# Kernel optimization log

Measured on AMD Instinct MI355X. Metric: run time of the kernel, lower is better.

## Reference

```python
import jax, jax.numpy as jnp
import numpy as np

H, KVH, D = 32, 8, 128
HID = H * D
OP = H * D + 2 * KVH * D
T = 2048
LAYER_IDX = 8
LAMBDA_INIT = float(0.8 - 0.6 * np.exp(-0.3 * LAYER_IDX))
EPS = 1e-5


def setup_inputs() -> dict:
    key = jax.random.key(0)
    ks = jax.random.split(key, 10)
    s = 0.02
    return {
        "hidden_states": jax.random.normal(ks[0], (T, HID), jnp.float32),
        "wqkv_w": jax.random.normal(ks[1], (OP, HID), jnp.float32) * s,
        "wqkv_b": jax.random.normal(ks[2], (OP,), jnp.float32) * s,
        "lambda_q1": jax.random.normal(ks[3], (D,), jnp.float32) * 0.1,
        "lambda_k1": jax.random.normal(ks[4], (D,), jnp.float32) * 0.1,
        "lambda_q2": jax.random.normal(ks[5], (D,), jnp.float32) * 0.1,
        "lambda_k2": jax.random.normal(ks[6], (D,), jnp.float32) * 0.1,
        "subln_w": jnp.ones((2 * D,), jnp.float32),
        "out_w": jax.random.normal(ks[7], (HID, HID), jnp.float32) * s,
        "out_b": jax.random.normal(ks[8], (HID,), jnp.float32) * s,
    }


def reference(hidden_states, wqkv_w, wqkv_b, lambda_q1, lambda_k1,
              lambda_q2, lambda_k2, subln_w, out_w, out_b):
    t = hidden_states.shape[0]
    scale = D ** -0.5

    qkv = hidden_states @ wqkv_w.T + wqkv_b                     # [T, OP]
    q, k, v = jnp.split(qkv, [H * D, H * D + KVH * D], axis=-1)

    # pair-wise head split: consecutive heads form (pair, component) groups
    q = q.reshape(t, H // 2, 2, D)                              # [T, Hp, 2, D]
    k = k.reshape(t, KVH // 2, 2, D)                            # [T, KVHp, 2, D]
    v = v.reshape(t, KVH // 2, 2 * D)                           # [T, KVHp, 2D]

    rep = H // KVH  # GQA: query pair p -> kv pair p // rep
    k = jnp.repeat(k, rep, axis=1)                              # [T, Hp, 2, D]
    v = jnp.repeat(v, rep, axis=1)                              # [T, Hp, 2D]

    lam = (jnp.exp(jnp.dot(lambda_q1, lambda_k1))
           - jnp.exp(jnp.dot(lambda_q2, lambda_k2)) + LAMBDA_INIT)

    causal = jnp.tril(jnp.ones((t, t), bool))
    scores = jnp.einsum('qhcd,khcd->hcqk', q, k) * scale        # [Hp, 2, T, T]
    scores = jnp.where(causal, scores, -jnp.inf)
    probs = jax.nn.softmax(scores, axis=-1)
    attn = probs[:, 0] - lam * probs[:, 1]                      # [Hp, T, T]

    out = jnp.einsum('hqk,khd->qhd', attn, v)                   # [T, Hp, 2D]

    # per-head RMSNorm over 2D, scaled by (1 - lambda_init)
    rms = jax.lax.rsqrt(jnp.mean(out * out, axis=-1, keepdims=True) + EPS)
    out = out * rms * subln_w * (1.0 - LAMBDA_INIT)

    out = out.reshape(t, H * D)
    return out @ out_w.T + out_b
```

## Files before the change

kernel.cpp:

```cpp
#include <hip/hip_runtime.h>

#define TTOK 2048
#define HIDN 4096
#define OPD  6144
#define DH   128
#define VD   256
#define KOFF 4096
#define VOFF 5120

typedef short  s16x8 __attribute__((ext_vector_type(8)));
typedef unsigned short u16x8 __attribute__((ext_vector_type(8)));
typedef float  fx4   __attribute__((ext_vector_type(4)));

constexpr float LAM_INIT = 0.7455692280263534f;
constexpr float OML      = 1.0f - LAM_INIT;
constexpr float QKSCALE  = 0.08838834764831845f;
constexpr float RESCALE_THR = 8.0f;

__device__ __forceinline__ unsigned short f2bf(float f) {
  unsigned int u = __builtin_bit_cast(unsigned int, f);
  u += 0x7fffu + ((u >> 16) & 1u);
  return (unsigned short)(u >> 16);
}

__device__ __forceinline__ unsigned int cvtpk(float lo, float hi) {
  unsigned int r;
  asm("v_cvt_pk_bf16_f32 %0, %1, %2" : "=v"(r) : "v"(lo), "v"(hi));
  return r;
}

__device__ __forceinline__ void g2l16(const void* gsrc, void* ldst) {
  __builtin_amdgcn_global_load_lds(
      (const __attribute__((address_space(1))) unsigned int*)gsrc,
      (__attribute__((address_space(3))) unsigned int*)ldst, 16, 0, 0);
}

__global__ __launch_bounds__(256)
void cvt3(const float* __restrict__ s0, unsigned short* __restrict__ d0, int nb0,
          const float* __restrict__ s1, unsigned short* __restrict__ d1, int nb1,
          const float* __restrict__ s2, unsigned short* __restrict__ d2)
{
  const int b = blockIdx.x;
  const float* s; unsigned short* d; int base;
  if (b < nb0)            { s = s0; d = d0; base = b << 11; }
  else if (b < nb0 + nb1) { s = s1; d = d1; base = (b - nb0) << 11; }
  else                    { s = s2; d = d2; base = (b - nb0 - nb1) << 11; }
  const int i = base + (int)threadIdx.x * 8;
  const float4 a0 = *(const float4*)(s + i);
  const float4 a1 = *(const float4*)(s + i + 4);
  u16x8 v;
  v[0]=f2bf(a0.x); v[1]=f2bf(a0.y); v[2]=f2bf(a0.z); v[3]=f2bf(a0.w);
  v[4]=f2bf(a1.x); v[5]=f2bf(a1.y); v[6]=f2bf(a1.z); v[7]=f2bf(a1.w);
  *(u16x8*)(d + i) = v;
}

__global__ __launch_bounds__(256)
void reduce2(const float* __restrict__ p, const float* __restrict__ bias,
             float* __restrict__ out)
{
  const size_t i = ((size_t)blockIdx.x * 256 + threadIdx.x) * 4;
  const int col = (int)(i & (HIDN - 1));
  const float4 a = *(const float4*)(p + i);
  const float4 b = *(const float4*)(p + (size_t)TTOK * HIDN + i);
  const float4 c = *(const float4*)(bias + col);
  float4 r;
  r.x = a.x + b.x + c.x; r.y = a.y + b.y + c.y;
  r.z = a.z + b.z + c.z; r.w = a.w + b.w + c.w;
  *(float4*)(out + i) = r;
}

__global__ __launch_bounds__(512, 2)
void gemm1_qkv(const unsigned short* __restrict__ A, const unsigned short* __restrict__ B,
               const float* __restrict__ bias, unsigned short* __restrict__ qq,
               unsigned short* __restrict__ ctt)
{
  __shared__ __align__(16) unsigned short As[2][2][128 * 64];
  __shared__ __align__(16) unsigned short Bs[2][192 * 64];

  const int tid  = threadIdx.x;
  const int lane = tid & 63, wid = tid >> 6;
  const int wm = wid >> 1, wn = wid & 1;
  const int m0 = blockIdx.y * 256, n0 = blockIdx.x * 192;
  const int l15 = lane & 15, lg = lane >> 4;

  const int scol = ((tid & 7) ^ ((tid >> 3) & 7)) << 3;
  const int rsw = (l15 & 7) << 3;
  const int ck0 = (lg * 8) ^ rsw;
  const int ck1 = (32 + lg * 8) ^ rsw;
  const int arh = wm * 16 + l15;
  const int brh = wn * 96 + l15;

  auto stageAh = [&](int kt, int buf, int h) {
    #pragma unroll
    for (int i = 0; i < 2; ++i) {
      const int li = i * 512 + tid;
      g2l16(A + (size_t)(m0 + h * 128 + (li >> 3)) * HIDN + kt + scol,
            &As[buf][h][li * 8]);
    }
  };
  auto stageB = [&](int kt, int buf) {
    #pragma unroll
    for (int i = 0; i < 3; ++i) {
      const int li = i * 512 + tid;
      g2l16(B + (size_t)(n0 + (li >> 3)) * HIDN + kt + scol,
            &Bs[buf][li * 8]);
    }
  };

  fx4 acc[4][6] = {};

  const int nk = HIDN >> 6;
  stageAh(0, 0, 0); stageB(0, 0); stageAh(0, 0, 1);
  asm volatile("s_waitcnt vmcnt(0)" ::: "memory");
  __builtin_amdgcn_s_barrier();

  for (int t = 0; t < nk; ++t) {
    const int buf = t & 1, nb = buf ^ 1;
    const int kt1 = (t + 1) << 6;
    const bool pre = (t + 1) < nk;
    const unsigned short* A0 = &As[buf][0][0];
    const unsigned short* A1 = &As[buf][1][0];
    const unsigned short* Bp = &Bs[buf][0];
    s16x8 af[2], bk0[6], bk1[6];

    af[0] = *(const s16x8*)&A0[(arh)      * 64 + ck0];
    af[1] = *(const s16x8*)&A0[(arh + 64) * 64 + ck0];
    #pragma unroll
    for (int n = 0; n < 6; ++n)
      bk0[n] = *(const s16x8*)&Bp[(brh + n * 16) * 64 + ck0];
    if (pre) {
      stageAh(kt1, nb, 0);
      asm volatile("s_waitcnt vmcnt(2)" ::: "memory");
    } else {
      asm volatile("s_waitcnt vmcnt(0)" ::: "memory");
    }
    __builtin_amdgcn_s_barrier();
    __builtin_amdgcn_s_setprio(1);
    #pragma unroll
    for (int m = 0; m < 2; ++m)
      #pragma unroll
      for (int n = 0; n < 6; ++n)
        acc[m][n] = __builtin_amdgcn_mfma_f32_16x16x32_bf16(af[m], bk0[n], acc[m][n], 0, 0, 0);
    __builtin_amdgcn_s_setprio(0);

    af[0] = *(const s16x8*)&A0[(arh)      * 64 + ck1];
    af[1] = *(const s16x8*)&A0[(arh + 64) * 64 + ck1];
    #pragma unroll
    for (int n = 0; n < 6; ++n)
      bk1[n] = *(const s16x8*)&Bp[(brh + n * 16) * 64 + ck1];
    if (pre) stageB(kt1, nb);
    __builtin_amdgcn_s_barrier();
    __builtin_amdgcn_s_setprio(1);
    #pragma unroll
    for (int m = 0; m < 2; ++m)
      #pragma unroll
      for (int n = 0; n < 6; ++n)
        acc[m][n] = __builtin_amdgcn_mfma_f32_16x16x32_bf16(af[m], bk1[n], acc[m][n], 0, 0, 0);
    __builtin_amdgcn_s_setprio(0);

    af[0] = *(const s16x8*)&A1[(arh)      * 64 + ck0];
    af[1] = *(const s16x8*)&A1[(arh + 64) * 64 + ck0];
    if (pre) stageAh(kt1, nb, 1);
    __builtin_amdgcn_s_setprio(1);
    #pragma unroll
    for (int m = 0; m < 2; ++m)
      #pragma unroll
      for (int n = 0; n < 6; ++n)
        acc[2 + m][n] = __builtin_amdgcn_mfma_f32_16x16x32_bf16(af[m], bk0[n], acc[2 + m][n], 0, 0, 0);
    __builtin_amdgcn_s_setprio(0);

    af[0] = *(const s16x8*)&A1[(arh)      * 64 + ck1];
    af[1] = *(const s16x8*)&A1[(arh + 64) * 64 + ck1];
    __builtin_amdgcn_s_setprio(1);
    #pragma unroll
    for (int m = 0; m < 2; ++m)
      #pragma unroll
      for (int n = 0; n < 6; ++n)
        acc[2 + m][n] = __builtin_amdgcn_mfma_f32_16x16x32_bf16(af[m], bk1[n], acc[2 + m][n], 0, 0, 0);
    __builtin_amdgcn_s_setprio(0);
  }

  #pragma unroll
  for (int mi = 0; mi < 4; ++mi)
    #pragma unroll
    for (int ni = 0; ni < 6; ++ni) {
      const int colg = n0 + wn * 96 + ni * 16;
      const int col  = colg + l15;
      const float bv = bias[col];
      const fx4 a = acc[mi][ni];
      const int row0 = m0 + mi * 64 + wm * 16 + lg * 4;
      if (colg >= VOFF) {
        ushort4 pk;
        pk.x = f2bf(a[0] + bv); pk.y = f2bf(a[1] + bv);
        pk.z = f2bf(a[2] + bv); pk.w = f2bf(a[3] + bv);
        const int d = col - VOFF;
        const int kvp = d >> 8, dw = d & 255;
        const int kt2 = row0 >> 5, kk = row0 & 31;
        const int kc = kk >> 3, k8 = kk & 7;
        *(ushort4*)&ctt[(size_t)kvp * 1048576 + (size_t)kt2 * 16384 + 8192
                        + kc * 2048 + dw * 8 + k8] = pk;
      } else if (colg >= KOFF) {
        const int ccol = col - KOFF;
        const int kvp = ccol >> 8, cw = ccol & 255;
        const int cc = cw >> 3, cbt = cw & 7;
        #pragma unroll
        for (int jj = 0; jj < 4; ++jj) {
          const int row2 = row0 + jj;
          const int kt2 = row2 >> 5, kk = row2 & 31;
          ctt[(size_t)kvp * 1048576 + (size_t)kt2 * 16384 + cc * 256 + kk * 8 + cbt]
              = f2bf(a[jj] + bv);
        }
      } else {
        #pragma unroll
        for (int jj = 0; jj < 4; ++jj)
          qq[(size_t)(row0 + jj) * HIDN + col] = f2bf((a[jj] + bv) * QKSCALE);
      }
    }
}

__global__ __launch_bounds__(512, 2)
void gemm2_sk(const unsigned short* __restrict__ A, const unsigned short* __restrict__ B,
              float* __restrict__ P, int K, int lda, int ldb, int ldc)
{
  __shared__ __align__(16) unsigned short As[2][2][128 * 64];
  __shared__ __align__(16) unsigned short Bs[2][2][128 * 64];

  const int tid  = threadIdx.x;
  const int lane = tid & 63, wid = tid >> 6;
  const int wm = wid >> 2, wn = wid & 3;
  const int m0 = blockIdx.y * 256, n0 = blockIdx.x * 256;
  const int l15 = lane & 15, lg = lane >> 4;
  const int kOff = blockIdx.z * K;

  const int scol = ((tid & 7) ^ ((tid >> 3) & 7)) << 3;
  const int rsw = (l15 & 7) << 3;
  const int ck0 = (lg * 8) ^ rsw;
  const int ck1 = (32 + lg * 8) ^ rsw;
  const int arh = wm * 16 + l15;
  const int brh = wn * 16 + l15;

  auto stageAh = [&](int kt, int buf, int h) {
    #pragma unroll
    for (int i = 0; i < 2; ++i) {
      const int li = i * 512 + tid;
      g2l16(A + (size_t)(m0 + h * 128 + (li >> 3)) * lda + kOff + kt + scol,
            &As[buf][h][li * 8]);
    }
  };
  auto stageBh = [&](int kt, int buf, int h) {
    #pragma unroll
    for (int i = 0; i < 2; ++i) {
      const int li = i * 512 + tid;
      g2l16(B + (size_t)(n0 + h * 128 + (li >> 3)) * ldb + kOff + kt + scol,
            &Bs[buf][h][li * 8]);
    }
  };

  fx4 acc[8][4] = {};

  const int nk = K >> 6;
  stageAh(0, 0, 0); stageBh(0, 0, 0); stageBh(0, 0, 1); stageAh(0, 0, 1);
  asm volatile("s_waitcnt vmcnt(0)" ::: "memory");
  __builtin_amdgcn_s_barrier();

  for (int t = 0; t < nk; ++t) {
    const int buf = t & 1, nb = buf ^ 1;
    const int kt1 = (t + 1) << 6;
    const bool pre = (t + 1) < nk;
    const unsigned short* A0 = &As[buf][0][0];
    const unsigned short* A1 = &As[buf][1][0];
    const unsigned short* B0 = &Bs[buf][0][0];
    const unsigned short* B1 = &Bs[buf][1][0];
    s16x8 af[4][2], bf0[2][2], bf1[2][2];

    #pragma unroll
    for (int m = 0; m < 4; ++m) {
      af[m][0] = *(const s16x8*)&A0[(arh + m * 32) * 64 + ck0];
      af[m][1] = *(const s16x8*)&A0[(arh + m * 32) * 64 + ck1];
    }
    #pragma unroll
    for (int n = 0; n < 2; ++n) {
      bf0[n][0] = *(const s16x8*)&B0[(brh + n * 64) * 64 + ck0];
      bf0[n][1] = *(const s16x8*)&B0[(brh + n * 64) * 64 + ck1];
    }
    if (pre) {
      stageAh(kt1, nb, 0);
      asm volatile("s_waitcnt vmcnt(4)" ::: "memory");
    } else {
      asm volatile("s_waitcnt vmcnt(0)" ::: "memory");
    }
    __builtin_amdgcn_s_barrier();
    __builtin_amdgcn_s_setprio(1);
    #pragma unroll
    for (int m = 0; m < 4; ++m)
      #pragma unroll
      for (int n = 0; n < 2; ++n) {
        acc[m][n] = __builtin_amdgcn_mfma_f32_16x16x32_bf16(af[m][0], bf0[n][0], acc[m][n], 0, 0, 0);
        acc[m][n] = __builtin_amdgcn_mfma_f32_16x16x32_bf16(af[m][1], bf0[n][1], acc[m][n], 0, 0, 0);
      }
    __builtin_amdgcn_s_setprio(0);

    #pragma unroll
    for (int n = 0; n < 2; ++n) {
      bf1[n][0] = *(const s16x8*)&B1[(brh + n * 64) * 64 + ck0];
      bf1[n][1] = *(const s16x8*)&B1[(brh + n * 64) * 64 + ck1];
    }
    if (pre) {
      stageBh(kt1, nb, 0);
      asm volatile("s_waitcnt vmcnt(4)" ::: "memory");
    }
    __builtin_amdgcn_s_barrier();
    __builtin_amdgcn_s_setprio(1);
    #pragma unroll
    for (int m = 0; m < 4; ++m)
      #pragma unroll
      for (int n = 0; n < 2; ++n) {
        acc[m][2 + n] = __builtin_amdgcn_mfma_f32_16x16x32_bf16(af[m][0], bf1[n][0], acc[m][2 + n], 0, 0, 0);
        acc[m][2 + n] = __builtin_amdgcn_mfma_f32_16x16x32_bf16(af[m][1], bf1[n][1], acc[m][2 + n], 0, 0, 0);
      }
    __builtin_amdgcn_s_setprio(0);

    #pragma unroll
    for (int m = 0; m < 4; ++m) {
      af[m][0] = *(const s16x8*)&A1[(arh + m * 32) * 64 + ck0];
      af[m][1] = *(const s16x8*)&A1[(arh + m * 32) * 64 + ck1];
    }
    if (pre) stageBh(kt1, nb, 1);
    __builtin_amdgcn_s_setprio(1);
    #pragma unroll
    for (int m = 0; m < 4; ++m)
      #pragma unroll
      for (int n = 0; n < 2; ++n) {
        acc[4 + m][2 + n] = __builtin_amdgcn_mfma_f32_16x16x32_bf16(af[m][0], bf1[n][0], acc[4 + m][2 + n], 0, 0, 0);
        acc[4 + m][2 + n] = __builtin_amdgcn_mfma_f32_16x16x32_bf16(af[m][1], bf1[n][1], acc[4 + m][2 + n], 0, 0, 0);
      }
    __builtin_amdgcn_s_setprio(0);

    if (pre) stageAh(kt1, nb, 1);
    __builtin_amdgcn_s_setprio(1);
    #pragma unroll
    for (int m = 0; m < 4; ++m)
      #pragma unroll
      for (int n = 0; n < 2; ++n) {
        acc[4 + m][n] = __builtin_amdgcn_mfma_f32_16x16x32_bf16(af[m][0], bf0[n][0], acc[4 + m][n], 0, 0, 0);
        acc[4 + m][n] = __builtin_amdgcn_mfma_f32_16x16x32_bf16(af[m][1], bf0[n][1], acc[4 + m][n], 0, 0, 0);
      }
    __builtin_amdgcn_s_setprio(0);
    if (pre) asm volatile("s_waitcnt vmcnt(4)" ::: "memory");
    __builtin_amdgcn_s_barrier();
  }

  float* Pz = P + (size_t)blockIdx.z * TTOK * ldc;
  const int rb = m0 + wm * 16;
  const int cb = n0 + wn * 16;
  #pragma unroll
  for (int mi = 0; mi < 8; ++mi)
    #pragma unroll
    for (int ni = 0; ni < 4; ++ni) {
      const int col = cb + ni * 64 + l15;
      const fx4 a = acc[mi][ni];
      #pragma unroll
      for (int jj = 0; jj < 4; ++jj)
        Pz[(size_t)(rb + mi * 32 + lg * 4 + jj) * ldc + col] = a[jj];
    }
}

__global__ __launch_bounds__(256, 2)
void attn_kernel(const unsigned short* __restrict__ qq,
                 const unsigned short* __restrict__ ctt,
                 const float* __restrict__ lq1, const float* __restrict__ lk1,
                 const float* __restrict__ lq2, const float* __restrict__ lk2,
                 const float* __restrict__ subln,
                 unsigned short* __restrict__ attn_out)
{
  __shared__ __align__(16) unsigned short Sb[2][16384];
  __shared__ __align__(16) unsigned short Pl[4][2][640];
  const int tid = threadIdx.x;
  const int lane = tid & 63, w = tid >> 6;
  const int l15 = lane & 15, lg = lane >> 4;

  const int bid  = blockIdx.x;
  const int r    = bid & 255;
  const int pair = r & 15;
  const int x    = r >> 4;
  const int qb   = (bid >> 8) ? x : 31 - x;
  const int kvp  = pair >> 2;
  const int q0b  = qb * 64;
  const int q0w  = q0b + w * 16;
  const int nt   = 2 * qb + 2;

  const unsigned short* cbase = ctt + (size_t)kvp * 1048576;

  auto stage = [&](int kt, int buf) {
    const unsigned short* src = cbase + (size_t)kt * 16384;
    const int off = w * 512 + lane * 8;
    #pragma unroll
    for (int i = 0; i < 8; ++i) {
      const int o = i * 2048 + off;
      g2l16(src + o, &Sb[buf][o]);
    }
  };

  stage(0, 0);

  float a1 = lq1[lane] * lk1[lane] + lq1[lane + 64] * lk1[lane + 64];
  float a2 = lq2[lane] * lk2[lane] + lq2[lane + 64] * lk2[lane + 64];
  #pragma unroll
  for (int sft = 1; sft < 64; sft <<= 1) { a1 += __shfl_xor(a1, sft); a2 += __shfl_xor(a2, sft); }
  const float lam = __expf(a1) - __expf(a2) + LAM_INIT;

  s16x8 qf0[4], qf1[4];
  {
    const unsigned short* qbp = qq + (size_t)(q0w + l15) * HIDN + pair * VD + lg * 8;
    #pragma unroll
    for (int kf = 0; kf < 4; ++kf) {
      qf0[kf] = *(const s16x8*)(qbp + kf * 32);
      qf1[kf] = *(const s16x8*)(qbp + DH + kf * 32);
    }
  }

  float mrun0 = -1e30f, mrun1 = -1e30f;
  float lrun0 = 0.f, lrun1 = 0.f;
  fx4 oacc0[16] = {}, oacc1[16] = {};
  unsigned short* pl0 = &Pl[w][0][0];
  unsigned short* pl1 = &Pl[w][1][0];
  const int q = q0w + l15;
  const int qmax = q0w + 15;

  for (int t = 0; t < nt; ++t) {
    __syncthreads();
    if (t + 1 < nt) stage(t + 1, (t + 1) & 1);
    const int kb = t * 32;
    if (kb > qmax) continue;
    const unsigned short* Kl = Sb[t & 1];
    const unsigned short* Vl = Sb[t & 1] + 8192;

    fx4 s00 = {0,0,0,0}, s01 = {0,0,0,0}, s10 = {0,0,0,0}, s11 = {0,0,0,0};
    #pragma unroll
    for (int kf = 0; kf < 4; ++kf) {
      const int cc0 = kf * 4 + lg;
      const int cc1 = 16 + kf * 4 + lg;
      const s16x8 k00 = *(const s16x8*)&Kl[cc0 * 256 + l15 * 8];
      const s16x8 k01 = *(const s16x8*)&Kl[cc0 * 256 + (16 + l15) * 8];
      const s16x8 k10 = *(const s16x8*)&Kl[cc1 * 256 + l15 * 8];
      const s16x8 k11 = *(const s16x8*)&Kl[cc1 * 256 + (16 + l15) * 8];
      s00 = __builtin_amdgcn_mfma_f32_16x16x32_bf16(k00, qf0[kf], s00, 0, 0, 0);
      s01 = __builtin_amdgcn_mfma_f32_16x16x32_bf16(k01, qf0[kf], s01, 0, 0, 0);
      s10 = __builtin_amdgcn_mfma_f32_16x16x32_bf16(k10, qf1[kf], s10, 0, 0, 0);
      s11 = __builtin_amdgcn_mfma_f32_16x16x32_bf16(k11, qf1[kf], s11, 0, 0, 0);
    }

    float v0[8], v1[8];
    if (kb + 32 <= q0w) {
      #pragma unroll
      for (int j = 0; j < 4; ++j) {
        v0[j] = s00[j]; v0[4 + j] = s01[j];
        v1[j] = s10[j]; v1[4 + j] = s11[j];
      }
    } else {
      #pragma unroll
      for (int j = 0; j < 4; ++j) {
        const int klo = kb + lg * 4 + j, khi = klo + 16;
        v0[j]     = (klo <= q) ? s00[j] : -1e30f;
        v0[4 + j] = (khi <= q) ? s01[j] : -1e30f;
        v1[j]     = (klo <= q) ? s10[j] : -1e30f;
        v1[4 + j] = (khi <= q) ? s11[j] : -1e30f;
      }
    }
    float tm0 = fmaxf(fmaxf(fmaxf(v0[0],v0[1]),fmaxf(v0[2],v0[3])),
                      fmaxf(fmaxf(v0[4],v0[5]),fmaxf(v0[6],v0[7])));
    float tm1 = fmaxf(fmaxf(fmaxf(v1[0],v1[1]),fmaxf(v1[2],v1[3])),
                      fmaxf(fmaxf(v1[4],v1[5]),fmaxf(v1[6],v1[7])));
    tm0 = fmaxf(tm0, __shfl_xor(tm0, 16)); tm0 = fmaxf(tm0, __shfl_xor(tm0, 32));
    tm1 = fmaxf(tm1, __shfl_xor(tm1, 16)); tm1 = fmaxf(tm1, __shfl_xor(tm1, 32));

    const bool need = (tm0 > mrun0 + RESCALE_THR) || (tm1 > mrun1 + RESCALE_THR);
    if (__any(need)) {
      const float mn0 = fmaxf(mrun0, tm0), mn1 = fmaxf(mrun1, tm1);
      const float fac0 = __expf(mrun0 - mn0), fac1 = __expf(mrun1 - mn1);
      mrun0 = mn0; mrun1 = mn1;
      lrun0 *= fac0; lrun1 *= fac1;
      #pragma unroll
      for (int jj = 0; jj < 4; ++jj) {
        const float fr0 = __shfl(fac0, lg * 4 + jj);
        const float fr1 = __shfl(fac1, lg * 4 + jj);
        #pragma unroll
        for (int nf = 0; nf < 16; ++nf) { oacc0[nf][jj] *= fr0; oacc1[nf][jj] *= fr1; }
      }
    }

    {
      float e0[8], e1[8];
      #pragma unroll
      for (int j = 0; j < 8; ++j) {
        e0[j] = __expf(v0[j] - mrun0);
        e1[j] = __expf(v1[j] - mrun1);
      }
      lrun0 += ((e0[0]+e0[1])+(e0[2]+e0[3])) + ((e0[4]+e0[5])+(e0[6]+e0[7]));
      lrun1 += ((e1[0]+e1[1])+(e1[2]+e1[3])) + ((e1[4]+e1[5])+(e1[6]+e1[7]));
      uint2 lo0, hi0, lo1, hi1;
      lo0.x = cvtpk(e0[0], e0[1]); lo0.y = cvtpk(e0[2], e0[3]);
      hi0.x = cvtpk(e0[4], e0[5]); hi0.y = cvtpk(e0[6], e0[7]);
      lo1.x = cvtpk(e1[0], e1[1]); lo1.y = cvtpk(e1[2], e1[3]);
      hi1.x = cvtpk(e1[4], e1[5]); hi1.y = cvtpk(e1[6], e1[7]);
      *(uint2*)&pl0[l15 * 40 + lg * 4]      = lo0;
      *(uint2*)&pl0[l15 * 40 + 16 + lg * 4] = hi0;
      *(uint2*)&pl1[l15 * 40 + lg * 4]      = lo1;
      *(uint2*)&pl1[l15 * 40 + 16 + lg * 4] = hi1;
    }
    asm volatile("s_waitcnt lgkmcnt(0)" ::: "memory");
    __builtin_amdgcn_sched_barrier(0);

    const s16x8 pa0 = *(const s16x8*)&pl0[l15 * 40 + lg * 8];
    const s16x8 pa1 = *(const s16x8*)&pl1[l15 * 40 + lg * 8];
    #pragma unroll
    for (int nf = 0; nf < 16; ++nf) {
      const s16x8 vf = *(const s16x8*)&Vl[lg * 2048 + (nf * 16 + l15) * 8];
      oacc0[nf] = __builtin_amdgcn_mfma_f32_16x16x32_bf16(pa0, vf, oacc0[nf], 0, 0, 0);
      oacc1[nf] = __builtin_amdgcn_mfma_f32_16x16x32_bf16(pa1, vf, oacc1[nf], 0, 0, 0);
    }
  }

  lrun0 += __shfl_xor(lrun0, 16); lrun0 += __shfl_xor(lrun0, 32);
  lrun1 += __shfl_xor(lrun1, 16); lrun1 += __shfl_xor(lrun1, 32);

  float li0[4], li1[4];
  #pragma unroll
  for (int jj = 0; jj < 4; ++jj) {
    li0[jj] = 1.0f / __shfl(lrun0, lg * 4 + jj);
    li1[jj] = 1.0f / __shfl(lrun1, lg * 4 + jj);
  }

  float ss[4] = {0.f, 0.f, 0.f, 0.f};
  #pragma unroll
  for (int nf = 0; nf < 16; ++nf)
    #pragma unroll
    for (int jj = 0; jj < 4; ++jj) {
      const float o = oacc0[nf][jj] * li0[jj] - lam * oacc1[nf][jj] * li1[jj];
      oacc0[nf][jj] = o;
      ss[jj] += o * o;
    }
  #pragma unroll
  for (int jj = 0; jj < 4; ++jj) {
    ss[jj] += __shfl_xor(ss[jj], 1);
    ss[jj] += __shfl_xor(ss[jj], 2);
    ss[jj] += __shfl_xor(ss[jj], 4);
    ss[jj] += __shfl_xor(ss[jj], 8);
    ss[jj] = rsqrtf(ss[jj] * (1.0f / 256.0f) + 1e-5f) * OML;
  }
  #pragma unroll
  for (int nf = 0; nf < 16; ++nf) {
    const int dcol = nf * 16 + l15;
    const float sw = subln[dcol];
    #pragma unroll
    for (int jj = 0; jj < 4; ++jj) {
      const int t = q0w + lg * 4 + jj;
      attn_out[(size_t)t * HIDN + pair * VD + dcol] = f2bf(oacc0[nf][jj] * ss[jj] * sw);
    }
  }
}

extern "C" void kernel_launch(void* const* d_in, const int* in_sizes, int n_in,
                              void* d_out, int out_size, void* d_ws, size_t ws_size,
                              hipStream_t stream) {
  (void)in_sizes; (void)n_in; (void)out_size; (void)ws_size;
  const float* hs     = (const float*)d_in[0];
  const float* wqkv_w = (const float*)d_in[1];
  const float* wqkv_b = (const float*)d_in[2];
  const float* lq1    = (const float*)d_in[3];
  const float* lk1    = (const float*)d_in[4];
  const float* lq2    = (const float*)d_in[5];
  const float* lk2    = (const float*)d_in[6];
  const float* subln  = (const float*)d_in[7];
  const float* out_w  = (const float*)d_in[8];
  const float* out_b  = (const float*)d_in[9];

  unsigned short* qq       = (unsigned short*)d_ws;
  unsigned short* ctt      = qq + (size_t)TTOK * HIDN;
  unsigned short* attn_out = ctt + (size_t)4 * 1048576;
  unsigned short* hs_bf    = attn_out + (size_t)TTOK * HIDN;
  unsigned short* wqkv_bf  = hs_bf + (size_t)TTOK * HIDN;
  unsigned short* outw_bf  = wqkv_bf + (size_t)OPD * HIDN;
  float*          partial  = (float*)hs_bf;

  const int nb0 = (TTOK * HIDN) >> 11;
  const int nb1 = (OPD * HIDN) >> 11;
  const int nb2 = (HIDN * HIDN) >> 11;
  cvt3<<<dim3(nb0 + nb1 + nb2), 256, 0, stream>>>(
      hs, hs_bf, nb0, wqkv_w, wqkv_bf, nb1, out_w, outw_bf);

  gemm1_qkv<<<dim3(OPD / 192, TTOK / 256), 512, 0, stream>>>(
      hs_bf, wqkv_bf, wqkv_b, qq, ctt);

  attn_kernel<<<dim3(512), 256, 0, stream>>>(
      qq, ctt, lq1, lk1, lq2, lk2, subln, attn_out);

  gemm2_sk<<<dim3(HIDN / 256, TTOK / 256, 2), 512, 0, stream>>>(
      attn_out, outw_bf, partial, HIDN / 2, HIDN, HIDN, HIDN);

  reduce2<<<dim3((TTOK * HIDN) / 1024), 256, 0, stream>>>(
      partial, out_b, (float*)d_out);
}
```

Baseline: 327.6 us.

## Fuse fp32-to-bf16 conversion into QKV GEMM loads, drop separate convert pass

The QKV GEMM now reads fp32 hidden states and weights directly into registers, converts them to bf16 and writes swizzled LDS tiles. This removes the separate conversion pass over hidden states and wqkv, along with its bf16 global writes and re-reads. The GEMM's staging changes from async global-to-LDS copies to a register-staged pipeline with one barrier per k-step. In exchange, every GEMM tile fetches fp32 data, which doubles global load bytes per tile and repeats the conversion across the blocks that share a tile, and the staging registers add pressure that may hurt occupancy.

New measurement: 342.1 us. 4.4% more time.

```diff
diff --git a/kernel.cpp b/kernel.cpp
--- a/kernel.cpp
+++ b/kernel.cpp
@@ -36,16 +36,9 @@
 }
 
 __global__ __launch_bounds__(256)
-void cvt3(const float* __restrict__ s0, unsigned short* __restrict__ d0, int nb0,
-          const float* __restrict__ s1, unsigned short* __restrict__ d1, int nb1,
-          const float* __restrict__ s2, unsigned short* __restrict__ d2)
+void cvt1(const float* __restrict__ s, unsigned short* __restrict__ d)
 {
-  const int b = blockIdx.x;
-  const float* s; unsigned short* d; int base;
-  if (b < nb0)            { s = s0; d = d0; base = b << 11; }
-  else if (b < nb0 + nb1) { s = s1; d = d1; base = (b - nb0) << 11; }
-  else                    { s = s2; d = d2; base = (b - nb0 - nb1) << 11; }
-  const int i = base + (int)threadIdx.x * 8;
+  const int i = (blockIdx.x << 11) + (int)threadIdx.x * 8;
   const float4 a0 = *(const float4*)(s + i);
   const float4 a1 = *(const float4*)(s + i + 4);
   u16x8 v;
@@ -70,7 +63,7 @@
 }
 
 __global__ __launch_bounds__(512, 2)
-void gemm1_qkv(const unsigned short* __restrict__ A, const unsigned short* __restrict__ B,
+void gemm1_qkv(const float* __restrict__ A, const float* __restrict__ B,
                const float* __restrict__ bias, unsigned short* __restrict__ qq,
                unsigned short* __restrict__ ctt)
 {
@@ -83,41 +76,68 @@
   const int m0 = blockIdx.y * 256, n0 = blockIdx.x * 192;
   const int l15 = lane & 15, lg = lane >> 4;
 
-  const int scol = ((tid & 7) ^ ((tid >> 3) & 7)) << 3;
+  const int srow = tid >> 3;
+  const int sc8  = (tid & 7) << 3;
+  const int swc  = (((tid & 7) ^ (srow & 7))) << 3;
   const int rsw = (l15 & 7) << 3;
   const int ck0 = (lg * 8) ^ rsw;
   const int ck1 = (32 + lg * 8) ^ rsw;
   const int arh = wm * 16 + l15;
   const int brh = wn * 96 + l15;
 
-  auto stageAh = [&](int kt, int buf, int h) {
-    #pragma unroll
-    for (int i = 0; i < 2; ++i) {
-      const int li = i * 512 + tid;
-      g2l16(A + (size_t)(m0 + h * 128 + (li >> 3)) * HIDN + kt + scol,
-            &As[buf][h][li * 8]);
+  fx4 la[2][2][2];
+  fx4 lb[3][2];
+
+  auto issueLoads = [&](int kt) {
+    #pragma unroll
+    for (int h = 0; h < 2; ++h)
+      #pragma unroll
+      for (int i = 0; i < 2; ++i) {
+        const float* ap = A + (size_t)(m0 + h * 128 + i * 64 + srow) * HIDN + kt + sc8;
+        la[h][i][0] = *(const fx4*)ap;
+        la[h][i][1] = *(const fx4*)(ap + 4);
+      }
+    #pragma unroll
+    for (int i = 0; i < 3; ++i) {
+      const float* bp = B + (size_t)(n0 + i * 64 + srow) * HIDN + kt + sc8;
+      lb[i][0] = *(const fx4*)bp;
+      lb[i][1] = *(const fx4*)(bp + 4);
     }
   };
-  auto stageB = [&](int kt, int buf) {
+  auto writeStage = [&](int buf) {
+    #pragma unroll
+    for (int h = 0; h < 2; ++h)
+      #pragma unroll
+      for (int i = 0; i < 2; ++i) {
+        uint4 w;
+        w.x = cvtpk(la[h][i][0][0], la[h][i][0][1]);
+        w.y = cvtpk(la[h][i][0][2], la[h][i][0][3]);
+        w.z = cvtpk(la[h][i][1][0], la[h][i][1][1]);
+        w.w = cvtpk(la[h][i][1][2], la[h][i][1][3]);
+        *(uint4*)&As[buf][h][(i * 64 + srow) * 64 + swc] = w;
+      }
     #pragma unroll
     for (int i = 0; i < 3; ++i) {
-      const int li = i * 512 + tid;
-      g2l16(B + (size_t)(n0 + (li >> 3)) * HIDN + kt + scol,
-            &Bs[buf][li * 8]);
+      uint4 w;
+      w.x = cvtpk(lb[i][0][0], lb[i][0][1]);
+      w.y = cvtpk(lb[i][0][2], lb[i][0][3]);
+      w.z = cvtpk(lb[i][1][0], lb[i][1][1]);
+      w.w = cvtpk(lb[i][1][2], lb[i][1][3]);
+      *(uint4*)&Bs[buf][(i * 64 + srow) * 64 + swc] = w;
     }
   };
 
   fx4 acc[4][6] = {};
 
   const int nk = HIDN >> 6;
-  stageAh(0, 0, 0); stageB(0, 0); stageAh(0, 0, 1);
-  asm volatile("s_waitcnt vmcnt(0)" ::: "memory");
+  issueLoads(0);
+  writeStage(0);
+  issueLoads(64);
+  asm volatile("s_waitcnt lgkmcnt(0)" ::: "memory");
   __builtin_amdgcn_s_barrier();
 
   for (int t = 0; t < nk; ++t) {
     const int buf = t & 1, nb = buf ^ 1;
-    const int kt1 = (t + 1) << 6;
-    const bool pre = (t + 1) < nk;
     const unsigned short* A0 = &As[buf][0][0];
     const unsigned short* A1 = &As[buf][1][0];
     const unsigned short* Bp = &Bs[buf][0];
@@ -128,13 +148,6 @@
     #pragma unroll
     for (int n = 0; n < 6; ++n)
       bk0[n] = *(const s16x8*)&Bp[(brh + n * 16) * 64 + ck0];
-    if (pre) {
-      stageAh(kt1, nb, 0);
-      asm volatile("s_waitcnt vmcnt(2)" ::: "memory");
-    } else {
-      asm volatile("s_waitcnt vmcnt(0)" ::: "memory");
-    }
-    __builtin_amdgcn_s_barrier();
     __builtin_amdgcn_s_setprio(1);
     #pragma unroll
     for (int m = 0; m < 2; ++m)
@@ -148,8 +161,6 @@
     #pragma unroll
     for (int n = 0; n < 6; ++n)
       bk1[n] = *(const s16x8*)&Bp[(brh + n * 16) * 64 + ck1];
-    if (pre) stageB(kt1, nb);
-    __builtin_amdgcn_s_barrier();
     __builtin_amdgcn_s_setprio(1);
     #pragma unroll
     for (int m = 0; m < 2; ++m)
@@ -160,7 +171,8 @@
 
     af[0] = *(const s16x8*)&A1[(arh)      * 64 + ck0];
     af[1] = *(const s16x8*)&A1[(arh + 64) * 64 + ck0];
-    if (pre) stageAh(kt1, nb, 1);
+    if (t + 1 < nk) writeStage(nb);
+    if (t + 2 < nk) issueLoads((t + 2) << 6);
     __builtin_amdgcn_s_setprio(1);
     #pragma unroll
     for (int m = 0; m < 2; ++m)
@@ -178,6 +190,11 @@
       for (int n = 0; n < 6; ++n)
         acc[2 + m][n] = __builtin_amdgcn_mfma_f32_16x16x32_bf16(af[m], bk1[n], acc[2 + m][n], 0, 0, 0);
     __builtin_amdgcn_s_setprio(0);
+
+    if (t + 1 < nk) {
+      asm volatile("s_waitcnt lgkmcnt(0)" ::: "memory");
+      __builtin_amdgcn_s_barrier();
+    }
   }
 
   #pragma unroll
@@ -578,19 +595,14 @@
   unsigned short* qq       = (unsigned short*)d_ws;
   unsigned short* ctt      = qq + (size_t)TTOK * HIDN;
   unsigned short* attn_out = ctt + (size_t)4 * 1048576;
-  unsigned short* hs_bf    = attn_out + (size_t)TTOK * HIDN;
-  unsigned short* wqkv_bf  = hs_bf + (size_t)TTOK * HIDN;
-  unsigned short* outw_bf  = wqkv_bf + (size_t)OPD * HIDN;
-  float*          partial  = (float*)hs_bf;
-
-  const int nb0 = (TTOK * HIDN) >> 11;
-  const int nb1 = (OPD * HIDN) >> 11;
-  const int nb2 = (HIDN * HIDN) >> 11;
-  cvt3<<<dim3(nb0 + nb1 + nb2), 256, 0, stream>>>(
-      hs, hs_bf, nb0, wqkv_w, wqkv_bf, nb1, out_w, outw_bf);
+  unsigned short* scratch  = attn_out + (size_t)TTOK * HIDN;
+  unsigned short* outw_bf  = scratch + (size_t)2 * TTOK * HIDN * 2;
+  float*          partial  = (float*)scratch;
+
+  cvt1<<<dim3((HIDN * HIDN) >> 11), 256, 0, stream>>>(out_w, outw_bf);
 
   gemm1_qkv<<<dim3(OPD / 192, TTOK / 256), 512, 0, stream>>>(
-      hs_bf, wqkv_bf, wqkv_b, qq, ctt);
+      hs, wqkv_w, wqkv_b, qq, ctt);
 
   attn_kernel<<<dim3(512), 256, 0, stream>>>(
       qq, ctt, lq1, lk1, lq2, lk2, subln, attn_out);
```

## Shrink QKV GEMM tile to 128x192 with 256 threads and simplify pipeline

Applied to the files above, without the earlier changes.

The QKV projection GEMM now uses 128-row block tiles with 4 waves instead of 256-row tiles with 8 waves. This doubles the grid to 512 blocks so the CUs are filled more evenly. Each wave now owns a contiguous 64x96 sub-tile. The prefetch schedule becomes a simpler two-stage double buffer with one barrier and a full vmcnt wait at the top of each k-step. In exchange, per-block operand reuse drops and the wait leaves less memory latency hidden.

Result: no change. 325.1 us (-0.8%).

```diff
diff --git a/kernel.cpp b/kernel.cpp
--- a/kernel.cpp
+++ b/kernel.cpp
@@ -69,114 +69,86 @@
   *(float4*)(out + i) = r;
 }
 
-__global__ __launch_bounds__(512, 2)
+__global__ __launch_bounds__(256, 2)
 void gemm1_qkv(const unsigned short* __restrict__ A, const unsigned short* __restrict__ B,
                const float* __restrict__ bias, unsigned short* __restrict__ qq,
                unsigned short* __restrict__ ctt)
 {
-  __shared__ __align__(16) unsigned short As[2][2][128 * 64];
+  __shared__ __align__(16) unsigned short As[2][128 * 64];
   __shared__ __align__(16) unsigned short Bs[2][192 * 64];
 
   const int tid  = threadIdx.x;
   const int lane = tid & 63, wid = tid >> 6;
   const int wm = wid >> 1, wn = wid & 1;
-  const int m0 = blockIdx.y * 256, n0 = blockIdx.x * 192;
+  const int m0 = blockIdx.y * 128, n0 = blockIdx.x * 192;
   const int l15 = lane & 15, lg = lane >> 4;
 
-  const int scol = ((tid & 7) ^ ((tid >> 3) & 7)) << 3;
+  const int srow = tid >> 3;
+  const int scol = ((tid & 7) ^ (srow & 7)) << 3;
   const int rsw = (l15 & 7) << 3;
   const int ck0 = (lg * 8) ^ rsw;
   const int ck1 = (32 + lg * 8) ^ rsw;
-  const int arh = wm * 16 + l15;
+  const int arh = wm * 64 + l15;
   const int brh = wn * 96 + l15;
 
-  auto stageAh = [&](int kt, int buf, int h) {
-    #pragma unroll
-    for (int i = 0; i < 2; ++i) {
-      const int li = i * 512 + tid;
-      g2l16(A + (size_t)(m0 + h * 128 + (li >> 3)) * HIDN + kt + scol,
-            &As[buf][h][li * 8]);
+  auto stageA = [&](int kt, int buf) {
+    #pragma unroll
+    for (int i = 0; i < 4; ++i) {
+      const int li = i * 256 + tid;
+      g2l16(A + (size_t)(m0 + (li >> 3)) * HIDN + kt + scol, &As[buf][li * 8]);
     }
   };
   auto stageB = [&](int kt, int buf) {
     #pragma unroll
-    for (int i = 0; i < 3; ++i) {
-      const int li = i * 512 + tid;
-      g2l16(B + (size_t)(n0 + (li >> 3)) * HIDN + kt + scol,
-            &Bs[buf][li * 8]);
+    for (int i = 0; i < 6; ++i) {
+      const int li = i * 256 + tid;
+      g2l16(B + (size_t)(n0 + (li >> 3)) * HIDN + kt + scol, &Bs[buf][li * 8]);
     }
   };
 
   fx4 acc[4][6] = {};
 
   const int nk = HIDN >> 6;
-  stageAh(0, 0, 0); stageB(0, 0); stageAh(0, 0, 1);
-  asm volatile("s_waitcnt vmcnt(0)" ::: "memory");
-  __builtin_amdgcn_s_barrier();
+  stageA(0, 0); stageB(0, 0);
 
   for (int t = 0; t < nk; ++t) {
     const int buf = t & 1, nb = buf ^ 1;
     const int kt1 = (t + 1) << 6;
     const bool pre = (t + 1) < nk;
-    const unsigned short* A0 = &As[buf][0][0];
-    const unsigned short* A1 = &As[buf][1][0];
+    const unsigned short* Ap = &As[buf][0];
     const unsigned short* Bp = &Bs[buf][0];
-    s16x8 af[2], bk0[6], bk1[6];
-
-    af[0] = *(const s16x8*)&A0[(arh)      * 64 + ck0];
-    af[1] = *(const s16x8*)&A0[(arh + 64) * 64 + ck0];
+    s16x8 af[4], bk[6];
+
+    asm volatile("s_waitcnt vmcnt(0)" ::: "memory");
+    __builtin_amdgcn_s_barrier();
+    if (pre) stageA(kt1, nb);
+    #pragma unroll
+    for (int m = 0; m < 4; ++m)
+      af[m] = *(const s16x8*)&Ap[(arh + m * 16) * 64 + ck0];
     #pragma unroll
     for (int n = 0; n < 6; ++n)
-      bk0[n] = *(const s16x8*)&Bp[(brh + n * 16) * 64 + ck0];
-    if (pre) {
-      stageAh(kt1, nb, 0);
-      asm volatile("s_waitcnt vmcnt(2)" ::: "memory");
-    } else {
-      asm volatile("s_waitcnt vmcnt(0)" ::: "memory");
-    }
-    __builtin_amdgcn_s_barrier();
+      bk[n] = *(const s16x8*)&Bp[(brh + n * 16) * 64 + ck0];
     __builtin_amdgcn_s_setprio(1);
     #pragma unroll
-    for (int m = 0; m < 2; ++m)
+    for (int m = 0; m < 4; ++m)
       #pragma unroll
       for (int n = 0; n < 6; ++n)
-        acc[m][n] = __builtin_amdgcn_mfma_f32_16x16x32_bf16(af[m], bk0[n], acc[m][n], 0, 0, 0);
+        acc[m][n] = __builtin_amdgcn_mfma_f32_16x16x32_bf16(af[m], bk[n], acc[m][n], 0, 0, 0);
     __builtin_amdgcn_s_setprio(0);
 
-    af[0] = *(const s16x8*)&A0[(arh)      * 64 + ck1];
-    af[1] = *(const s16x8*)&A0[(arh + 64) * 64 + ck1];
+    #pragma unroll
+    for (int m = 0; m < 4; ++m)
+      af[m] = *(const s16x8*)&Ap[(arh + m * 16) * 64 + ck1];
     #pragma unroll
     for (int n = 0; n < 6; ++n)
-      bk1[n] = *(const s16x8*)&Bp[(brh + n * 16) * 64 + ck1];
+      bk[n] = *(const s16x8*)&Bp[(brh + n * 16) * 64 + ck1];
     if (pre) stageB(kt1, nb);
-    __builtin_amdgcn_s_barrier();
     __builtin_amdgcn_s_setprio(1);
     #pragma unroll
-    for (int m = 0; m < 2; ++m)
+    for (int m = 0; m < 4; ++m)
       #pragma unroll
       for (int n = 0; n < 6; ++n)
-        acc[m][n] = __builtin_amdgcn_mfma_f32_16x16x32_bf16(af[m], bk1[n], acc[m][n], 0, 0, 0);
-    __builtin_amdgcn_s_setprio(0);
-
-    af[0] = *(const s16x8*)&A1[(arh)      * 64 + ck0];
-    af[1] = *(const s16x8*)&A1[(arh + 64) * 64 + ck0];
-    if (pre) stageAh(kt1, nb, 1);
-    __builtin_amdgcn_s_setprio(1);
-    #pragma unroll
-    for (int m = 0; m < 2; ++m)
-      #pragma unroll
-      for (int n = 0; n < 6; ++n)
-        acc[2 + m][n] = __builtin_amdgcn_mfma_f32_16x16x32_bf16(af[m], bk0[n], acc[2 + m][n], 0, 0, 0);
-    __builtin_amdgcn_s_setprio(0);
-
-    af[0] = *(const s16x8*)&A1[(arh)      * 64 + ck1];
-    af[1] = *(const s16x8*)&A1[(arh + 64) * 64 + ck1];
-    __builtin_amdgcn_s_setprio(1);
-    #pragma unroll
-    for (int m = 0; m < 2; ++m)
-      #pragma unroll
-      for (int n = 0; n < 6; ++n)
-        acc[2 + m][n] = __builtin_amdgcn_mfma_f32_16x16x32_bf16(af[m], bk1[n], acc[2 + m][n], 0, 0, 0);
+        acc[m][n] = __builtin_amdgcn_mfma_f32_16x16x32_bf16(af[m], bk[n], acc[m][n], 0, 0, 0);
     __builtin_amdgcn_s_setprio(0);
   }
 
@@ -188,7 +160,7 @@
       const int col  = colg + l15;
       const float bv = bias[col];
       const fx4 a = acc[mi][ni];
-      const int row0 = m0 + mi * 64 + wm * 16 + lg * 4;
+      const int row0 = m0 + wm * 64 + mi * 16 + lg * 4;
       if (colg >= VOFF) {
         ushort4 pk;
         pk.x = f2bf(a[0] + bv); pk.y = f2bf(a[1] + bv);
@@ -589,7 +561,7 @@
   cvt3<<<dim3(nb0 + nb1 + nb2), 256, 0, stream>>>(
       hs, hs_bf, nb0, wqkv_w, wqkv_bf, nb1, out_w, outw_bf);
 
-  gemm1_qkv<<<dim3(OPD / 192, TTOK / 256), 512, 0, stream>>>(
+  gemm1_qkv<<<dim3(OPD / 192, TTOK / 128), 256, 0, stream>>>(
       hs_bf, wqkv_bf, wqkv_b, qq, ctt);
 
   attn_kernel<<<dim3(512), 256, 0, stream>>>(
```
